# Kernel optimization log

Measured on AMD Instinct MI355X. Metric: run time of the kernel, lower is better.

Reference implementation:

```python
import jax, jax.numpy as jnp
import numpy as np

HEADS = 8
DIM = 64      # dim
DH = 64       # dim_head
DK = 24       # dim_k (== dim_head_k * heads, required by reshape in forward)
DHK = 3       # dim_head_k (also conv groups)


def setup_inputs() -> dict:
    key = jax.random.key(0)
    ks = jax.random.split(key, 10)
    b, h, w = 4, 128, 128
    return {
        "x_in": jax.random.normal(ks[0], (b, h, w, DIM), jnp.float32),
        "illu_fea_trans": jax.random.normal(ks[1], (b, h, w, DIM), jnp.float32),
        "illu_map_trans": jax.random.normal(ks[2], (b, h, w, DK), jnp.float32),
        # Linear weights stored as [in, out] (torch stores [out, in]; math y = x @ W_in_out)
        "Wq": jax.random.normal(ks[3], (DIM, HEADS * DH), jnp.float32) * 0.05,
        "Wk": jax.random.normal(ks[4], (DK, HEADS * DHK), jnp.float32) * 0.05,
        "Wv": jax.random.normal(ks[5], (DIM, HEADS * DH), jnp.float32) * 0.05,
        "rescale": jnp.ones((HEADS, 1, 1), jnp.float32),
        "Wp": jax.random.normal(ks[6], (HEADS * DHK, DK), jnp.float32) * 0.05,
        "bp": jax.random.normal(ks[7], (DK,), jnp.float32) * 0.05,
        # grouped conv weights, OIHW: [out=24, in/groups=8, 3, 3]
        "conv1_w": jax.random.normal(ks[8], (DK, DK // DHK, 3, 3), jnp.float32) * 0.05,
        "conv2_w": jax.random.normal(ks[9], (DK, DK // DHK, 3, 3), jnp.float32) * 0.05,
    }


def _gconv(x_nchw, w_oihw):
    return jax.lax.conv_general_dilated(
        x_nchw, w_oihw, window_strides=(1, 1), padding='SAME',
        feature_group_count=DHK,
        dimension_numbers=('NCHW', 'OIHW', 'NCHW'))


def reference(x_in, illu_fea_trans, illu_map_trans, Wq, Wk, Wv, rescale, Wp, bp, conv1_w, conv2_w):
    b, h, w, c = x_in.shape
    n = h * w
    # projections
    q = (x_in.reshape(b, n, c) @ Wq).reshape(b, n, HEADS, DH)
    k_inp = illu_map_trans.reshape(b, n, DK) @ Wk            # [b, n, heads*dhk]
    v = (illu_fea_trans.reshape(b, n, c) @ Wv).reshape(b, n, HEADS, DH)
    kh = k_inp.reshape(b, n, HEADS, DHK)
    q = q / (DIM ** 0.5)  # note: scaled by sqrt(dim), not sqrt(dim_head)
    # channel-wise cross-attention: attn over channel dims, contracting tokens n
    attn = jnp.einsum('bnhk,bnhd->bhkd', kh, q) * rescale[None]  # [b, heads, dhk, dh]
    attn = jax.nn.softmax(attn, axis=-1)
    out = jnp.einsum('bhkd,bnhd->bnkh', attn, v)             # [b, n, dhk, heads]
    out = out.reshape(b, n, DHK * HEADS) @ Wp + bp           # proj
    out = out.reshape(b, h, w, DK)
    # positional branch: two grouped 3x3 convs with exact GELU on k_inp
    kx = k_inp.reshape(b, h, w, DK).transpose(0, 3, 1, 2)    # NCHW
    y = _gconv(kx, conv1_w)
    y = jax.nn.gelu(y, approximate=False)
    y = _gconv(y, conv2_w)
    return out + y.transpose(0, 2, 3, 1)
```

## Files before the change

kernel.cpp:

```cpp
#include <hip/hip_runtime.h>
#include <math.h>

#define HEADS 8
#define DIM   64
#define DK    24
#define DHK   3
#define BB    4
#define HH    128
#define WW    128
#define NN    (HH*WW)
#define QSCALE 0.125f

__global__ __launch_bounds__(256) void s_reduce(
    const float* __restrict__ imap,
    const float* __restrict__ x,
    float* __restrict__ Sp_part)
{
    __shared__ float part[4*1536];
    const int tid = threadIdx.x;
    const int blk = blockIdx.x;
    const int b = blk >> 6, chunk = blk & 63;
    const int w = tid >> 6, lane = tid & 63;
    const int cq = lane & 15;
    const int ig = lane >> 4;

    const long tok0 = (long)b * NN + chunk * 256 + w * 64;
    const float* xp = x    + tok0 * 64 + cq * 4;
    const float* mp = imap + tok0 * 24 + ig * 6;

    float acc[6][4];
    #pragma unroll
    for (int r = 0; r < 6; ++r)
        #pragma unroll
        for (int q = 0; q < 4; ++q) acc[r][q] = 0.f;

    for (int t = 0; t < 64; ++t) {
        float4 xv = *(const float4*)(xp + t * 64);
        float2 m0 = *(const float2*)(mp + t * 24);
        float2 m1 = *(const float2*)(mp + t * 24 + 2);
        float2 m2 = *(const float2*)(mp + t * 24 + 4);
        float mm[6] = {m0.x, m0.y, m1.x, m1.y, m2.x, m2.y};
        #pragma unroll
        for (int r = 0; r < 6; ++r) {
            acc[r][0] += mm[r] * xv.x;
            acc[r][1] += mm[r] * xv.y;
            acc[r][2] += mm[r] * xv.z;
            acc[r][3] += mm[r] * xv.w;
        }
    }

    float* pp = part + w * 1536;
    #pragma unroll
    for (int r = 0; r < 6; ++r) {
        float4 v = {acc[r][0], acc[r][1], acc[r][2], acc[r][3]};
        *(float4*)(pp + (ig * 6 + r) * 64 + cq * 4) = v;
    }
    __syncthreads();

    for (int e = tid; e < 1536; e += 256)
        Sp_part[(long)blk * 1536 + e] =
            part[e] + part[1536 + e] + part[3072 + e] + part[4608 + e];
}

__global__ __launch_bounds__(256) void attn_fused(
    const float* __restrict__ Sp_part,
    const float* __restrict__ Wk,
    const float* __restrict__ Wq,
    const float* __restrict__ Wv,
    const float* __restrict__ rescale,
    const float* __restrict__ Wp,
    float* __restrict__ Pt)
{
    __shared__ float Sp_l[1536];
    __shared__ float S_l[1536];
    __shared__ float att[1536];
    __shared__ float M_l[1536];

    const int b = blockIdx.x, tid = threadIdx.x;

    {
        float s[6] = {0.f, 0.f, 0.f, 0.f, 0.f, 0.f};
        const float* p = Sp_part + (long)b * 64 * 1536;
        for (int c0 = 0; c0 < 64; c0 += 8) {
            float v[8][6];
            #pragma unroll
            for (int cc = 0; cc < 8; ++cc)
                #pragma unroll
                for (int k = 0; k < 6; ++k)
                    v[cc][k] = p[(long)(c0 + cc) * 1536 + tid + 256 * k];
            #pragma unroll
            for (int cc = 0; cc < 8; ++cc)
                #pragma unroll
                for (int k = 0; k < 6; ++k)
                    s[k] += v[cc][k];
        }
        #pragma unroll
        for (int k = 0; k < 6; ++k) Sp_l[tid + 256 * k] = s[k];
    }
    __syncthreads();

    for (int q = tid; q < 1536; q += 256) {
        int c = q & 63, j = q >> 6;
        float s = 0.f;
        #pragma unroll
        for (int i = 0; i < 24; ++i) s += Wk[i * 24 + j] * Sp_l[i * 64 + c];
        S_l[q] = s;
    }
    __syncthreads();

    for (int q = tid; q < 1536; q += 256) {
        int d = q & 63, ch = q >> 6;
        int h = ch / 3;
        const float* wq = Wq + h * 64 + d;
        const float* sr = S_l + ch * 64;
        float s = 0.f;
        for (int cc = 0; cc < 64; ++cc) s += sr[cc] * wq[cc * 512];
        att[q] = s * QSCALE * rescale[h];
    }
    __syncthreads();

    if (tid < 24) {
        float* row = att + tid * 64;
        float mx = row[0];
        for (int d = 1; d < 64; ++d) mx = fmaxf(mx, row[d]);
        float sum = 0.f;
        for (int d = 0; d < 64; ++d) { float e = expf(row[d] - mx); row[d] = e; sum += e; }
        float inv = 1.f / sum;
        for (int d = 0; d < 64; ++d) row[d] *= inv;
    }
    __syncthreads();

    for (int q = tid; q < 1536; q += 256) {
        int c = q & 63, ch = q >> 6;
        int h = ch / 3;
        const float* wv = Wv + c * 512 + h * 64;
        const float* ar = att + ch * 64;
        float s = 0.f;
        for (int d = 0; d < 64; ++d) s += ar[d] * wv[d];
        M_l[ch * 64 + c] = s;
    }
    __syncthreads();

    for (int q = tid; q < 1536; q += 256) {
        int c = q & 63, jo = q >> 6;
        float s = 0.f;
        #pragma unroll
        for (int k = 0; k < 3; ++k)
            #pragma unroll
            for (int h = 0; h < 8; ++h)
                s += M_l[(h * 3 + k) * 64 + c] * Wp[(k * 8 + h) * 24 + jo];
        Pt[b * 1536 + q] = s;
    }
}

__global__ __launch_bounds__(192, 2) void conv_fused(
    const float* __restrict__ imap, const float* __restrict__ Wk,
    const float* __restrict__ c1w,  const float* __restrict__ fea,
    const float* __restrict__ c2w,  const float* __restrict__ Pt,
    const float* __restrict__ bp,   float* __restrict__ outp)
{
    __shared__ __align__(16) float kbuf[144 * 28];
    __shared__ __align__(16) float y1l[100 * 28];

    const int tid = threadIdx.x;
    const int blk = blockIdx.x;
    const int b = blk >> 8, ti = (blk >> 4) & 15, tj = blk & 15;
    const int i0 = ti * 8, j0 = tj * 8;
    const int o = tid % 24, jj = tid / 24;
    const int g = o >> 3;

    if (tid < 144) {
        const int pi = tid / 12, pj = tid % 12;
        const int gi = i0 + pi - 2, gj = j0 + pj - 2;
        float kv[24];
        #pragma unroll
        for (int j = 0; j < 24; ++j) kv[j] = 0.f;
        if (gi >= 0 && gi < HH && gj >= 0 && gj < WW) {
            const float4* m4 = (const float4*)(imap + (((long)b * HH + gi) * WW + gj) * 24);
            float m[24];
            #pragma unroll
            for (int i = 0; i < 6; ++i) {
                float4 v = m4[i];
                m[4*i+0]=v.x; m[4*i+1]=v.y; m[4*i+2]=v.z; m[4*i+3]=v.w;
            }
            for (int i = 0; i < 24; ++i) {
                float mi = m[i];
                #pragma unroll
                for (int j = 0; j < 24; ++j) kv[j] += mi * Wk[i * 24 + j];
            }
        }
        #pragma unroll
        for (int j = 0; j < 24; ++j) kbuf[tid * 28 + j] = kv[j];
    }
    __syncthreads();

    {
        float wr[8][9];
        {
            const float4* wp = (const float4*)(c1w + o * 72);
            #pragma unroll
            for (int t = 0; t < 18; ++t) ((float4*)wr)[t] = wp[t];
        }
        for (int task = tid; task < 240; task += 192) {
            const int r = task / 24;
            float wc[3][3][8];
            #pragma unroll
            for (int slot = 0; slot < 2; ++slot)
                #pragma unroll
                for (int di = 0; di < 3; ++di) {
                    const float* p = kbuf + ((r + di) * 12 + slot) * 28 + g * 8;
                    *(float4*)&wc[slot][di][0] = *(const float4*)(p);
                    *(float4*)&wc[slot][di][4] = *(const float4*)(p + 4);
                }
            #pragma unroll
            for (int c = 0; c < 10; ++c) {
                const int s2 = (c + 2) % 3;
                #pragma unroll
                for (int di = 0; di < 3; ++di) {
                    const float* p = kbuf + ((r + di) * 12 + (c + 2)) * 28 + g * 8;
                    *(float4*)&wc[s2][di][0] = *(const float4*)(p);
                    *(float4*)&wc[s2][di][4] = *(const float4*)(p + 4);
                }
                float s = 0.f;
                #pragma unroll
                for (int dj = 0; dj < 3; ++dj) {
                    const int sl = (c + dj) % 3;
                    #pragma unroll
                    for (int di = 0; di < 3; ++di)
                        #pragma unroll
                        for (int ic = 0; ic < 8; ++ic)
                            s += wc[sl][di][ic] * wr[ic][di * 3 + dj];
                }
                const int gi = i0 + r - 1, gj = j0 + c - 1;
                float val = 0.f;
                if (gi >= 0 && gi < HH && gj >= 0 && gj < WW)
                    val = 0.5f * s * (1.f + erff(s * 0.70710678f));
                y1l[(r * 10 + c) * 28 + o] = val;
            }
        }
    }
    __syncthreads();

    float wr[8][9];
    {
        const float4* wp = (const float4*)(c2w + o * 72);
        #pragma unroll
        for (int t = 0; t < 18; ++t) ((float4*)wr)[t] = wp[t];
    }

    float acc[8];
    {
        const float bo = bp[o];
        #pragma unroll
        for (int ii = 0; ii < 8; ++ii) acc[ii] = bo;
        const float* PtRow = Pt + b * 1536 + o * 64;
        const float* feaB = fea + (((long)(b * HH + i0)) * WW + (j0 + jj)) * 64;
        for (int cq = 0; cq < 16; ++cq) {
            float4 p = *(const float4*)(PtRow + cq * 4);
            #pragma unroll
            for (int ii = 0; ii < 8; ++ii) {
                float4 f = *(const float4*)(feaB + (long)ii * WW * 64 + cq * 4);
                acc[ii] += f.x * p.x + f.y * p.y + f.z * p.z + f.w * p.w;
            }
        }
    }

    float win[3][3][8];
    #define LROW(R, SLOT)                                                     \
    {                                                                         \
        const float* rp_ = y1l + ((R) * 10 + jj) * 28 + g * 8;                \
        *(float4*)&win[SLOT][0][0] = *(const float4*)(rp_);                   \
        *(float4*)&win[SLOT][0][4] = *(const float4*)(rp_ + 4);               \
        *(float4*)&win[SLOT][1][0] = *(const float4*)(rp_ + 28);              \
        *(float4*)&win[SLOT][1][4] = *(const float4*)(rp_ + 32);              \
        *(float4*)&win[SLOT][2][0] = *(const float4*)(rp_ + 56);              \
        *(float4*)&win[SLOT][2][4] = *(const float4*)(rp_ + 60);              \
    }

    LROW(0, 0)
    LROW(1, 1)
    #pragma unroll
    for (int ii = 0; ii < 8; ++ii) {
        LROW(ii + 2, (ii + 2) % 3)
        float s = 0.f;
        #pragma unroll
        for (int di = 0; di < 3; ++di) {
            const int slot = (ii + di) % 3;
            #pragma unroll
            for (int dj = 0; dj < 3; ++dj)
                #pragma unroll
                for (int ic = 0; ic < 8; ++ic)
                    s += win[slot][dj][ic] * wr[ic][di * 3 + dj];
        }
        outp[((long)((b * HH + i0 + ii) * WW + j0)) * 24 + tid] = acc[ii] + s;
    }
    #undef LROW
}

extern "C" void kernel_launch(void* const* d_in, const int* in_sizes, int n_in,
                              void* d_out, int out_size, void* d_ws, size_t ws_size,
                              hipStream_t stream) {
    const float* x_in    = (const float*)d_in[0];
    const float* fea     = (const float*)d_in[1];
    const float* imap    = (const float*)d_in[2];
    const float* Wq      = (const float*)d_in[3];
    const float* Wk      = (const float*)d_in[4];
    const float* Wv      = (const float*)d_in[5];
    const float* rescale = (const float*)d_in[6];
    const float* Wp      = (const float*)d_in[7];
    const float* bp      = (const float*)d_in[8];
    const float* c1w     = (const float*)d_in[9];
    const float* c2w     = (const float*)d_in[10];
    float* out = (float*)d_out;

    float* ws      = (float*)d_ws;
    float* Sp_part = ws;
    float* Pt      = ws + 393216;

    s_reduce<<<256, 256, 0, stream>>>(imap, x_in, Sp_part);
    attn_fused<<<4, 256, 0, stream>>>(Sp_part, Wk, Wq, Wv, rescale, Wp, Pt);
    conv_fused<<<BB * 256, 192, 0, stream>>>(imap, Wk, c1w, fea, c2w, Pt, bp, out);
}
```

Baseline: 177.2 us.

## Parallelize attention per head and reduce partial sums with atomics

The token reduction now runs on 1024 blocks of 16 tokens per wave and accumulates directly into a per-batch buffer with atomicAdd, replacing the partial-sum buffer and its serial reduction in the attention kernel. The attention kernel is split into 32 blocks (one per batch and head), using a wave-level shuffle softmax and an LDS-staged slice of Wv, and it accumulates the projection output with atomics. A memset is added to zero the accumulators. The aim is to remove the heavily serial 4-block attention kernel and the large partial-buffer traffic, at the cost of atomic contention, nondeterministic summation order and an extra memset launch.

Measured after the change: 159.2 us. 10.1% less time.

```diff
diff --git a/kernel.cpp b/kernel.cpp
--- a/kernel.cpp
+++ b/kernel.cpp
@@ -14,17 +14,17 @@
 __global__ __launch_bounds__(256) void s_reduce(
     const float* __restrict__ imap,
     const float* __restrict__ x,
-    float* __restrict__ Sp_part)
+    float* __restrict__ Sp)
 {
     __shared__ float part[4*1536];
     const int tid = threadIdx.x;
     const int blk = blockIdx.x;
-    const int b = blk >> 6, chunk = blk & 63;
+    const int b = blk >> 8, chunk = blk & 255;
     const int w = tid >> 6, lane = tid & 63;
     const int cq = lane & 15;
     const int ig = lane >> 4;
 
-    const long tok0 = (long)b * NN + chunk * 256 + w * 64;
+    const long tok0 = (long)b * NN + chunk * 64 + w * 16;
     const float* xp = x    + tok0 * 64 + cq * 4;
     const float* mp = imap + tok0 * 24 + ig * 6;
 
@@ -34,7 +34,8 @@
         #pragma unroll
         for (int q = 0; q < 4; ++q) acc[r][q] = 0.f;
 
-    for (int t = 0; t < 64; ++t) {
+    #pragma unroll 4
+    for (int t = 0; t < 16; ++t) {
         float4 xv = *(const float4*)(xp + t * 64);
         float2 m0 = *(const float2*)(mp + t * 24);
         float2 m1 = *(const float2*)(mp + t * 24 + 2);
@@ -58,12 +59,12 @@
     __syncthreads();
 
     for (int e = tid; e < 1536; e += 256)
-        Sp_part[(long)blk * 1536 + e] =
-            part[e] + part[1536 + e] + part[3072 + e] + part[4608 + e];
+        atomicAdd(&Sp[b * 1536 + e],
+                  part[e] + part[1536 + e] + part[3072 + e] + part[4608 + e]);
 }
 
-__global__ __launch_bounds__(256) void attn_fused(
-    const float* __restrict__ Sp_part,
+__global__ __launch_bounds__(192) void attn_fused(
+    const float* __restrict__ Sp,
     const float* __restrict__ Wk,
     const float* __restrict__ Wq,
     const float* __restrict__ Wv,
@@ -72,84 +73,66 @@
     float* __restrict__ Pt)
 {
     __shared__ float Sp_l[1536];
-    __shared__ float S_l[1536];
-    __shared__ float att[1536];
-    __shared__ float M_l[1536];
-
-    const int b = blockIdx.x, tid = threadIdx.x;
-
-    {
-        float s[6] = {0.f, 0.f, 0.f, 0.f, 0.f, 0.f};
-        const float* p = Sp_part + (long)b * 64 * 1536;
-        for (int c0 = 0; c0 < 64; c0 += 8) {
-            float v[8][6];
-            #pragma unroll
-            for (int cc = 0; cc < 8; ++cc)
-                #pragma unroll
-                for (int k = 0; k < 6; ++k)
-                    v[cc][k] = p[(long)(c0 + cc) * 1536 + tid + 256 * k];
-            #pragma unroll
-            for (int cc = 0; cc < 8; ++cc)
-                #pragma unroll
-                for (int k = 0; k < 6; ++k)
-                    s[k] += v[cc][k];
-        }
-        #pragma unroll
-        for (int k = 0; k < 6; ++k) Sp_l[tid + 256 * k] = s[k];
-    }
-    __syncthreads();
-
-    for (int q = tid; q < 1536; q += 256) {
-        int c = q & 63, j = q >> 6;
+    __shared__ float sS[192];
+    __shared__ float sP[192];
+    __shared__ float Wv_l[64 * 65];
+
+    const int tid = threadIdx.x, blk = blockIdx.x;
+    const int b = blk >> 3, h = blk & 7;
+    const int k3 = tid >> 6, lane = tid & 63;
+
+    for (int e = tid; e < 1536; e += 192) Sp_l[e] = Sp[b * 1536 + e];
+    for (int e = tid; e < 4096; e += 192) {
+        int c = e >> 6, d = e & 63;
+        Wv_l[c * 65 + d] = Wv[c * 512 + h * 64 + d];
+    }
+    __syncthreads();
+
+    {
+        const float* wk = Wk + (h * 3 + k3);
         float s = 0.f;
         #pragma unroll
-        for (int i = 0; i < 24; ++i) s += Wk[i * 24 + j] * Sp_l[i * 64 + c];
-        S_l[q] = s;
-    }
-    __syncthreads();
-
-    for (int q = tid; q < 1536; q += 256) {
-        int d = q & 63, ch = q >> 6;
-        int h = ch / 3;
-        const float* wq = Wq + h * 64 + d;
-        const float* sr = S_l + ch * 64;
-        float s = 0.f;
-        for (int cc = 0; cc < 64; ++cc) s += sr[cc] * wq[cc * 512];
-        att[q] = s * QSCALE * rescale[h];
-    }
-    __syncthreads();
-
-    if (tid < 24) {
-        float* row = att + tid * 64;
-        float mx = row[0];
-        for (int d = 1; d < 64; ++d) mx = fmaxf(mx, row[d]);
-        float sum = 0.f;
-        for (int d = 0; d < 64; ++d) { float e = expf(row[d] - mx); row[d] = e; sum += e; }
-        float inv = 1.f / sum;
-        for (int d = 0; d < 64; ++d) row[d] *= inv;
-    }
-    __syncthreads();
-
-    for (int q = tid; q < 1536; q += 256) {
-        int c = q & 63, ch = q >> 6;
-        int h = ch / 3;
-        const float* wv = Wv + c * 512 + h * 64;
-        const float* ar = att + ch * 64;
-        float s = 0.f;
-        for (int d = 0; d < 64; ++d) s += ar[d] * wv[d];
-        M_l[ch * 64 + c] = s;
-    }
-    __syncthreads();
-
-    for (int q = tid; q < 1536; q += 256) {
-        int c = q & 63, jo = q >> 6;
-        float s = 0.f;
+        for (int i = 0; i < 24; ++i) s += wk[i * 24] * Sp_l[i * 64 + lane];
+        sS[k3 * 64 + lane] = s;
+    }
+    __syncthreads();
+
+    {
+        const float* wq = Wq + h * 64 + lane;
+        const float* sr = sS + k3 * 64;
+        float a = 0.f;
+        for (int c = 0; c < 64; ++c) a += sr[c] * wq[c * 512];
+        a *= QSCALE * rescale[h];
+        float mx = a;
+        #pragma unroll
+        for (int off = 32; off >= 1; off >>= 1)
+            mx = fmaxf(mx, __shfl_xor(mx, off, 64));
+        float e = expf(a - mx);
+        float sum = e;
+        #pragma unroll
+        for (int off = 32; off >= 1; off >>= 1)
+            sum += __shfl_xor(sum, off, 64);
+        sP[k3 * 64 + lane] = e / sum;
+    }
+    __syncthreads();
+
+    {
+        const float* pr = sP + k3 * 64;
+        const float* wv = Wv_l + lane * 65;
+        float m = 0.f;
+        #pragma unroll
+        for (int d = 0; d < 64; ++d) m += pr[d] * wv[d];
+        sS[k3 * 64 + lane] = m;
+    }
+    __syncthreads();
+
+    for (int q = tid; q < 1536; q += 192) {
+        int o = q >> 6, c = q & 63;
+        float v = 0.f;
         #pragma unroll
         for (int k = 0; k < 3; ++k)
-            #pragma unroll
-            for (int h = 0; h < 8; ++h)
-                s += M_l[(h * 3 + k) * 64 + c] * Wp[(k * 8 + h) * 24 + jo];
-        Pt[b * 1536 + q] = s;
+            v += sS[k * 64 + c] * Wp[(k * 8 + h) * 24 + o];
+        atomicAdd(&Pt[b * 1536 + o * 64 + c], v);
     }
 }
 
@@ -313,11 +296,12 @@
     const float* c2w     = (const float*)d_in[10];
     float* out = (float*)d_out;
 
-    float* ws      = (float*)d_ws;
-    float* Sp_part = ws;
-    float* Pt      = ws + 393216;
-
-    s_reduce<<<256, 256, 0, stream>>>(imap, x_in, Sp_part);
-    attn_fused<<<4, 256, 0, stream>>>(Sp_part, Wk, Wq, Wv, rescale, Wp, Pt);
+    float* ws = (float*)d_ws;
+    float* Sp = ws;
+    float* Pt = ws + 6144;
+
+    hipMemsetAsync(ws, 0, 12288 * sizeof(float), stream);
+    s_reduce<<<1024, 256, 0, stream>>>(imap, x_in, Sp);
+    attn_fused<<<32, 192, 0, stream>>>(Sp, Wk, Wq, Wv, rescale, Wp, Pt);
     conv_fused<<<BB * 256, 192, 0, stream>>>(imap, Wk, c1w, fea, c2w, Pt, bp, out);
 }
```

## Fuse reduction and attention via last-block counter; double threads in conv kernel

Applied to the files above, without the earlier changes.

The token reduction and the per-batch attention computation now run in one kernel. Each block writes its partial sums, and an atomic counter elects the last block per batch to finish the attention math, with a wave-shuffle softmax replacing the serial one. This removes a kernel launch and the tiny 4-block serial attention stage, at the cost of a memset launch and a fence. The conv kernel doubles its threads to 384 and splits the k projection, conv1 and output rows across more threads for more parallelism per tile.

Result: slower. 226.6 us (+27.9%).

```diff
diff --git a/kernel.cpp b/kernel.cpp
--- a/kernel.cpp
+++ b/kernel.cpp
@@ -11,12 +11,21 @@
 #define NN    (HH*WW)
 #define QSCALE 0.125f
 
-__global__ __launch_bounds__(256) void s_reduce(
+__global__ __launch_bounds__(512) void reduce_attn(
     const float* __restrict__ imap,
     const float* __restrict__ x,
-    float* __restrict__ Sp_part)
+    const float* __restrict__ Wk,
+    const float* __restrict__ Wq,
+    const float* __restrict__ Wv,
+    const float* __restrict__ rescale,
+    const float* __restrict__ Wp,
+    float* __restrict__ Sp_part,
+    float* __restrict__ Pt,
+    int* __restrict__ cnt)
 {
-    __shared__ float part[4*1536];
+    __shared__ float buf[8 * 1540];
+    __shared__ int isLast;
+
     const int tid = threadIdx.x;
     const int blk = blockIdx.x;
     const int b = blk >> 6, chunk = blk & 63;
@@ -24,136 +33,135 @@
     const int cq = lane & 15;
     const int ig = lane >> 4;
 
-    const long tok0 = (long)b * NN + chunk * 256 + w * 64;
-    const float* xp = x    + tok0 * 64 + cq * 4;
-    const float* mp = imap + tok0 * 24 + ig * 6;
-
-    float acc[6][4];
-    #pragma unroll
-    for (int r = 0; r < 6; ++r)
-        #pragma unroll
-        for (int q = 0; q < 4; ++q) acc[r][q] = 0.f;
-
-    for (int t = 0; t < 64; ++t) {
-        float4 xv = *(const float4*)(xp + t * 64);
-        float2 m0 = *(const float2*)(mp + t * 24);
-        float2 m1 = *(const float2*)(mp + t * 24 + 2);
-        float2 m2 = *(const float2*)(mp + t * 24 + 4);
-        float mm[6] = {m0.x, m0.y, m1.x, m1.y, m2.x, m2.y};
+    {
+        const long tok0 = (long)b * NN + chunk * 256 + w * 32;
+        const float* xp = x    + tok0 * 64 + cq * 4;
+        const float* mp = imap + tok0 * 24 + ig * 6;
+
+        float acc[6][4];
+        #pragma unroll
+        for (int r = 0; r < 6; ++r)
+            #pragma unroll
+            for (int q = 0; q < 4; ++q) acc[r][q] = 0.f;
+
+        #pragma unroll 4
+        for (int t = 0; t < 32; ++t) {
+            float4 xv = *(const float4*)(xp + t * 64);
+            float2 m0 = *(const float2*)(mp + t * 24);
+            float2 m1 = *(const float2*)(mp + t * 24 + 2);
+            float2 m2 = *(const float2*)(mp + t * 24 + 4);
+            float mm[6] = {m0.x, m0.y, m1.x, m1.y, m2.x, m2.y};
+            #pragma unroll
+            for (int r = 0; r < 6; ++r) {
+                acc[r][0] += mm[r] * xv.x;
+                acc[r][1] += mm[r] * xv.y;
+                acc[r][2] += mm[r] * xv.z;
+                acc[r][3] += mm[r] * xv.w;
+            }
+        }
+
+        float* pp = buf + w * 1540;
         #pragma unroll
         for (int r = 0; r < 6; ++r) {
-            acc[r][0] += mm[r] * xv.x;
-            acc[r][1] += mm[r] * xv.y;
-            acc[r][2] += mm[r] * xv.z;
-            acc[r][3] += mm[r] * xv.w;
-        }
-    }
-
-    float* pp = part + w * 1536;
-    #pragma unroll
-    for (int r = 0; r < 6; ++r) {
-        float4 v = {acc[r][0], acc[r][1], acc[r][2], acc[r][3]};
-        *(float4*)(pp + (ig * 6 + r) * 64 + cq * 4) = v;
-    }
-    __syncthreads();
-
-    for (int e = tid; e < 1536; e += 256)
-        Sp_part[(long)blk * 1536 + e] =
-            part[e] + part[1536 + e] + part[3072 + e] + part[4608 + e];
-}
-
-__global__ __launch_bounds__(256) void attn_fused(
-    const float* __restrict__ Sp_part,
-    const float* __restrict__ Wk,
-    const float* __restrict__ Wq,
-    const float* __restrict__ Wv,
-    const float* __restrict__ rescale,
-    const float* __restrict__ Wp,
-    float* __restrict__ Pt)
-{
-    __shared__ float Sp_l[1536];
-    __shared__ float S_l[1536];
-    __shared__ float att[1536];
-    __shared__ float M_l[1536];
-
-    const int b = blockIdx.x, tid = threadIdx.x;
-
-    {
-        float s[6] = {0.f, 0.f, 0.f, 0.f, 0.f, 0.f};
-        const float* p = Sp_part + (long)b * 64 * 1536;
-        for (int c0 = 0; c0 < 64; c0 += 8) {
-            float v[8][6];
-            #pragma unroll
-            for (int cc = 0; cc < 8; ++cc)
-                #pragma unroll
-                for (int k = 0; k < 6; ++k)
-                    v[cc][k] = p[(long)(c0 + cc) * 1536 + tid + 256 * k];
-            #pragma unroll
-            for (int cc = 0; cc < 8; ++cc)
-                #pragma unroll
-                for (int k = 0; k < 6; ++k)
-                    s[k] += v[cc][k];
-        }
-        #pragma unroll
-        for (int k = 0; k < 6; ++k) Sp_l[tid + 256 * k] = s[k];
-    }
-    __syncthreads();
-
-    for (int q = tid; q < 1536; q += 256) {
-        int c = q & 63, j = q >> 6;
-        float s = 0.f;
-        #pragma unroll
-        for (int i = 0; i < 24; ++i) s += Wk[i * 24 + j] * Sp_l[i * 64 + c];
-        S_l[q] = s;
-    }
-    __syncthreads();
-
-    for (int q = tid; q < 1536; q += 256) {
-        int d = q & 63, ch = q >> 6;
-        int h = ch / 3;
+            float4 v = {acc[r][0], acc[r][1], acc[r][2], acc[r][3]};
+            *(float4*)(pp + (ig * 6 + r) * 64 + cq * 4) = v;
+        }
+    }
+    __syncthreads();
+
+    for (int e = tid; e < 1536; e += 512) {
+        float s = 0.f;
+        #pragma unroll
+        for (int ww = 0; ww < 8; ++ww) s += buf[ww * 1540 + e];
+        Sp_part[(long)blk * 1536 + e] = s;
+    }
+
+    __threadfence();
+    __syncthreads();
+    if (tid == 0) {
+        int old = atomicAdd(&cnt[b], 1);
+        isLast = (old == 63);
+    }
+    __syncthreads();
+    if (!isLast) return;
+    __threadfence();
+
+    float* Sp_l = buf;
+    float* S_l  = buf + 1536;
+    float* att  = buf + 3072;
+    float* M_l  = buf + 4608;
+
+    for (int e = tid; e < 1536; e += 512) {
+        float s = 0.f;
+        const float* p = Sp_part + (long)(b * 64) * 1536 + e;
+        #pragma unroll 8
+        for (int pb = 0; pb < 64; ++pb) s += p[(long)pb * 1536];
+        Sp_l[e] = s;
+    }
+    __syncthreads();
+
+    for (int e = tid; e < 1536; e += 512) {
+        int c = e & 63, ch = e >> 6;
+        float s = 0.f;
+        #pragma unroll
+        for (int i = 0; i < 24; ++i) s += Wk[i * 24 + ch] * Sp_l[i * 64 + c];
+        S_l[e] = s;
+    }
+    __syncthreads();
+
+    for (int e = tid; e < 1536; e += 512) {
+        int d = e & 63, ch = e >> 6, h = ch / 3;
         const float* wq = Wq + h * 64 + d;
         const float* sr = S_l + ch * 64;
         float s = 0.f;
-        for (int cc = 0; cc < 64; ++cc) s += sr[cc] * wq[cc * 512];
-        att[q] = s * QSCALE * rescale[h];
-    }
-    __syncthreads();
-
-    if (tid < 24) {
-        float* row = att + tid * 64;
-        float mx = row[0];
-        for (int d = 1; d < 64; ++d) mx = fmaxf(mx, row[d]);
-        float sum = 0.f;
-        for (int d = 0; d < 64; ++d) { float e = expf(row[d] - mx); row[d] = e; sum += e; }
-        float inv = 1.f / sum;
-        for (int d = 0; d < 64; ++d) row[d] *= inv;
-    }
-    __syncthreads();
-
-    for (int q = tid; q < 1536; q += 256) {
-        int c = q & 63, ch = q >> 6;
-        int h = ch / 3;
+        for (int c2 = 0; c2 < 64; ++c2) s += sr[c2] * wq[c2 * 512];
+        att[e] = s * QSCALE * rescale[h];
+    }
+    __syncthreads();
+
+    {
+        #pragma unroll
+        for (int k = 0; k < 3; ++k) {
+            int r = w * 3 + k;
+            float a = att[r * 64 + lane];
+            float mx = a;
+            #pragma unroll
+            for (int off = 32; off >= 1; off >>= 1)
+                mx = fmaxf(mx, __shfl_xor(mx, off, 64));
+            float e = expf(a - mx);
+            float sum = e;
+            #pragma unroll
+            for (int off = 32; off >= 1; off >>= 1)
+                sum += __shfl_xor(sum, off, 64);
+            att[r * 64 + lane] = e / sum;
+        }
+    }
+    __syncthreads();
+
+    for (int e = tid; e < 1536; e += 512) {
+        int c = e & 63, ch = e >> 6, h = ch / 3;
+        const float* pr = att + ch * 64;
         const float* wv = Wv + c * 512 + h * 64;
-        const float* ar = att + ch * 64;
-        float s = 0.f;
-        for (int d = 0; d < 64; ++d) s += ar[d] * wv[d];
-        M_l[ch * 64 + c] = s;
-    }
-    __syncthreads();
-
-    for (int q = tid; q < 1536; q += 256) {
-        int c = q & 63, jo = q >> 6;
+        float s = 0.f;
+        #pragma unroll
+        for (int d = 0; d < 64; ++d) s += pr[d] * wv[d];
+        M_l[e] = s;
+    }
+    __syncthreads();
+
+    for (int e = tid; e < 1536; e += 512) {
+        int c = e & 63, o = e >> 6;
         float s = 0.f;
         #pragma unroll
         for (int k = 0; k < 3; ++k)
             #pragma unroll
             for (int h = 0; h < 8; ++h)
-                s += M_l[(h * 3 + k) * 64 + c] * Wp[(k * 8 + h) * 24 + jo];
-        Pt[b * 1536 + q] = s;
+                s += M_l[(h * 3 + k) * 64 + c] * Wp[(k * 8 + h) * 24 + o];
+        Pt[b * 1536 + e] = s;
     }
 }
 
-__global__ __launch_bounds__(192, 2) void conv_fused(
+__global__ __launch_bounds__(384) void conv_fused(
     const float* __restrict__ imap, const float* __restrict__ Wk,
     const float* __restrict__ c1w,  const float* __restrict__ fea,
     const float* __restrict__ c2w,  const float* __restrict__ Pt,
@@ -166,15 +174,17 @@
     const int blk = blockIdx.x;
     const int b = blk >> 8, ti = (blk >> 4) & 15, tj = blk & 15;
     const int i0 = ti * 8, j0 = tj * 8;
-    const int o = tid % 24, jj = tid / 24;
+    const int o = tid % 24;
     const int g = o >> 3;
-
-    if (tid < 144) {
-        const int pi = tid / 12, pj = tid % 12;
+    const int jj2 = tid / 24;
+
+    if (tid < 288) {
+        const int px = tid >> 1, half = tid & 1;
+        const int pi = px / 12, pj = px % 12;
         const int gi = i0 + pi - 2, gj = j0 + pj - 2;
-        float kv[24];
-        #pragma unroll
-        for (int j = 0; j < 24; ++j) kv[j] = 0.f;
+        float kv[12];
+        #pragma unroll
+        for (int j = 0; j < 12; ++j) kv[j] = 0.f;
         if (gi >= 0 && gi < HH && gj >= 0 && gj < WW) {
             const float4* m4 = (const float4*)(imap + (((long)b * HH + gi) * WW + gj) * 24);
             float m[24];
@@ -186,11 +196,11 @@
             for (int i = 0; i < 24; ++i) {
                 float mi = m[i];
                 #pragma unroll
-                for (int j = 0; j < 24; ++j) kv[j] += mi * Wk[i * 24 + j];
-            }
-        }
-        #pragma unroll
-        for (int j = 0; j < 24; ++j) kbuf[tid * 28 + j] = kv[j];
+                for (int j = 0; j < 12; ++j) kv[j] += mi * Wk[i * 24 + half * 12 + j];
+            }
+        }
+        #pragma unroll
+        for (int j = 0; j < 12; ++j) kbuf[px * 28 + half * 12 + j] = kv[j];
     }
     __syncthreads();
 
@@ -201,46 +211,49 @@
             #pragma unroll
             for (int t = 0; t < 18; ++t) ((float4*)wr)[t] = wp[t];
         }
-        for (int task = tid; task < 240; task += 192) {
-            const int r = task / 24;
+        for (int task = tid; task < 480; task += 384) {
+            const int r = task / 48;
+            const int half = (task / 24) & 1;
+            const int c0 = half * 5;
             float wc[3][3][8];
             #pragma unroll
             for (int slot = 0; slot < 2; ++slot)
                 #pragma unroll
                 for (int di = 0; di < 3; ++di) {
-                    const float* p = kbuf + ((r + di) * 12 + slot) * 28 + g * 8;
+                    const float* p = kbuf + ((r + di) * 12 + c0 + slot) * 28 + g * 8;
                     *(float4*)&wc[slot][di][0] = *(const float4*)(p);
                     *(float4*)&wc[slot][di][4] = *(const float4*)(p + 4);
                 }
             #pragma unroll
-            for (int c = 0; c < 10; ++c) {
-                const int s2 = (c + 2) % 3;
+            for (int c5 = 0; c5 < 5; ++c5) {
+                const int s2 = (c5 + 2) % 3;
                 #pragma unroll
                 for (int di = 0; di < 3; ++di) {
-                    const float* p = kbuf + ((r + di) * 12 + (c + 2)) * 28 + g * 8;
+                    const float* p = kbuf + ((r + di) * 12 + c0 + c5 + 2) * 28 + g * 8;
                     *(float4*)&wc[s2][di][0] = *(const float4*)(p);
                     *(float4*)&wc[s2][di][4] = *(const float4*)(p + 4);
                 }
                 float s = 0.f;
                 #pragma unroll
                 for (int dj = 0; dj < 3; ++dj) {
-                    const int sl = (c + dj) % 3;
+                    const int sl = (c5 + dj) % 3;
                     #pragma unroll
                     for (int di = 0; di < 3; ++di)
                         #pragma unroll
                         for (int ic = 0; ic < 8; ++ic)
                             s += wc[sl][di][ic] * wr[ic][di * 3 + dj];
                 }
-                const int gi = i0 + r - 1, gj = j0 + c - 1;
+                const int gi = i0 + r - 1, gj = j0 + c0 + c5 - 1;
                 float val = 0.f;
                 if (gi >= 0 && gi < HH && gj >= 0 && gj < WW)
                     val = 0.5f * s * (1.f + erff(s * 0.70710678f));
-                y1l[(r * 10 + c) * 28 + o] = val;
-            }
-        }
-    }
-    __syncthreads();
-
+                y1l[(r * 10 + c0 + c5) * 28 + o] = val;
+            }
+        }
+    }
+    __syncthreads();
+
+    const int jj = jj2 & 7, rh = jj2 >> 3;
     float wr[8][9];
     {
         const float4* wp = (const float4*)(c2w + o * 72);
@@ -248,19 +261,19 @@
         for (int t = 0; t < 18; ++t) ((float4*)wr)[t] = wp[t];
     }
 
-    float acc[8];
+    float acc[4];
     {
         const float bo = bp[o];
         #pragma unroll
-        for (int ii = 0; ii < 8; ++ii) acc[ii] = bo;
+        for (int lr = 0; lr < 4; ++lr) acc[lr] = bo;
         const float* PtRow = Pt + b * 1536 + o * 64;
-        const float* feaB = fea + (((long)(b * HH + i0)) * WW + (j0 + jj)) * 64;
+        const float* feaB = fea + (((long)(b * HH + i0 + rh * 4)) * WW + (j0 + jj)) * 64;
         for (int cq = 0; cq < 16; ++cq) {
             float4 p = *(const float4*)(PtRow + cq * 4);
             #pragma unroll
-            for (int ii = 0; ii < 8; ++ii) {
-                float4 f = *(const float4*)(feaB + (long)ii * WW * 64 + cq * 4);
-                acc[ii] += f.x * p.x + f.y * p.y + f.z * p.z + f.w * p.w;
+            for (int lr = 0; lr < 4; ++lr) {
+                float4 f = *(const float4*)(feaB + (long)lr * WW * 64 + cq * 4);
+                acc[lr] += f.x * p.x + f.y * p.y + f.z * p.z + f.w * p.w;
             }
         }
     }
@@ -277,22 +290,22 @@
         *(float4*)&win[SLOT][2][4] = *(const float4*)(rp_ + 60);              \
     }
 
-    LROW(0, 0)
-    LROW(1, 1)
+    LROW(rh * 4 + 0, 0)
+    LROW(rh * 4 + 1, 1)
     #pragma unroll
-    for (int ii = 0; ii < 8; ++ii) {
-        LROW(ii + 2, (ii + 2) % 3)
+    for (int lr = 0; lr < 4; ++lr) {
+        LROW(rh * 4 + lr + 2, (lr + 2) % 3)
         float s = 0.f;
         #pragma unroll
         for (int di = 0; di < 3; ++di) {
-            const int slot = (ii + di) % 3;
+            const int slot = (lr + di) % 3;
             #pragma unroll
             for (int dj = 0; dj < 3; ++dj)
                 #pragma unroll
                 for (int ic = 0; ic < 8; ++ic)
                     s += win[slot][dj][ic] * wr[ic][di * 3 + dj];
         }
-        outp[((long)((b * HH + i0 + ii) * WW + j0)) * 24 + tid] = acc[ii] + s;
+        outp[((long)((b * HH + i0 + rh * 4 + lr) * WW + j0 + jj)) * 24 + o] = acc[lr] + s;
     }
     #undef LROW
 }
@@ -316,8 +329,10 @@
     float* ws      = (float*)d_ws;
     float* Sp_part = ws;
     float* Pt      = ws + 393216;
-
-    s_reduce<<<256, 256, 0, stream>>>(imap, x_in, Sp_part);
-    attn_fused<<<4, 256, 0, stream>>>(Sp_part, Wk, Wq, Wv, rescale, Wp, Pt);
-    conv_fused<<<BB * 256, 192, 0, stream>>>(imap, Wk, c1w, fea, c2w, Pt, bp, out);
+    int*   cnt     = (int*)(ws + 399360);
+
+    hipMemsetAsync(cnt, 0, 4 * sizeof(int), stream);
+    reduce_attn<<<256, 512, 0, stream>>>(imap, x_in, Wk, Wq, Wv, rescale, Wp,
+                                         Sp_part, Pt, cnt);
+    conv_fused<<<BB * 256, 384, 0, stream>>>(imap, Wk, c1w, fea, c2w, Pt, bp, out);
 }
```
